# Kernel tuning notes

Measured on AMD Instinct MI355X. Metric: run time of the kernel, lower is better.

Reference implementation:

```python
import jax, jax.numpy as jnp
import numpy as np

V, E, H, T, B, D, L = 32000, 512, 512, 128, 4, 4, 2
C0, C1 = 2000, 10000          # adaptive softmax cutoffs
NT = T - D + 1


def setup_inputs() -> dict:
    key = jax.random.key(0)
    ks = jax.random.split(key, 18)
    s = 0.02
    x = jax.random.randint(ks[0], (B, T), 1, V)
    lengths = jnp.sort(jax.random.randint(ks[1], (B,), D, T + 1))[::-1]
    lengths = lengths.at[0].set(T)
    # graph predictor output: per-layer attention matrices [B, L, T, T]
    G = jax.nn.softmax(jax.random.normal(ks[2], (B, L, T, T)), axis=-1)
    emb = (jax.random.normal(ks[3], (V, E)) * s).at[0].set(0.0)  # padding_idx=0
    enc_w_ih = jax.random.normal(ks[4], (L, 3 * H, H)) * s
    enc_w_hh = jax.random.normal(ks[5], (L, 3 * H, H)) * s
    enc_b_ih = jnp.zeros((L, 3 * H))
    enc_b_hh = jnp.zeros((L, 3 * H))
    dec_w_ih = jax.random.normal(ks[6], (3 * H, E)) * s
    dec_w_hh = jax.random.normal(ks[7], (3 * H, H)) * s
    dec_b_ih = jnp.zeros((3 * H,))
    dec_b_hh = jnp.zeros((3 * H,))
    head_w = jax.random.normal(ks[8], (C0 + 2, H)) * s
    t0_proj = jax.random.normal(ks[9], (H // 4, H)) * s
    t0_out = jax.random.normal(ks[10], (C1 - C0, H // 4)) * s
    t1_proj = jax.random.normal(ks[11], (H // 16, H)) * s
    t1_out = jax.random.normal(ks[12], (V - C1, H // 16)) * s
    return dict(x=x, lengths=lengths, G=G, emb=emb,
                enc_w_ih=enc_w_ih, enc_w_hh=enc_w_hh, enc_b_ih=enc_b_ih, enc_b_hh=enc_b_hh,
                dec_w_ih=dec_w_ih, dec_w_hh=dec_w_hh, dec_b_ih=dec_b_ih, dec_b_hh=dec_b_hh,
                head_w=head_w, t0_proj=t0_proj, t0_out=t0_out, t1_proj=t1_proj, t1_out=t1_out)


def gru_step(xt, h, w_ih, w_hh, b_ih, b_hh):
    """torch nn.GRU/GRUCell math; works on arbitrary leading dims."""
    gi = xt @ w_ih.T + b_ih
    gh = h @ w_hh.T + b_hh
    i_r, i_z, i_n = jnp.split(gi, 3, axis=-1)
    h_r, h_z, h_n = jnp.split(gh, 3, axis=-1)
    r = jax.nn.sigmoid(i_r + h_r)
    z = jax.nn.sigmoid(i_z + h_z)
    n = jnp.tanh(i_n + r * h_n)
    return (1.0 - z) * n + z * h


def adaptive_log_prob(h, head_w, t0_proj, t0_out, t1_proj, t1_out):
    """torch AdaptiveLogSoftmaxWithLoss.log_prob: h [N,H] -> [N,V]."""
    head_lp = jax.nn.log_softmax(h @ head_w.T, axis=-1)                      # [N, C0+2]
    lp0 = head_lp[:, C0:C0 + 1] + jax.nn.log_softmax((h @ t0_proj.T) @ t0_out.T, axis=-1)
    lp1 = head_lp[:, C0 + 1:C0 + 2] + jax.nn.log_softmax((h @ t1_proj.T) @ t1_out.T, axis=-1)
    return jnp.concatenate([head_lp[:, :C0], lp0, lp1], axis=-1)


def reference(x, lengths, G, emb, enc_w_ih, enc_w_hh, enc_b_ih, enc_b_hh,
              dec_w_ih, dec_w_hh, dec_b_ih, dec_b_hh,
              head_w, t0_proj, t0_out, t1_proj, t1_out):
    b = x.shape[0]
    input_f = emb[x]                      # [B,T,E] (dropout p=0)
    embedded = input_f
    # ---- encoder: graph-weighted aggregation + GRUCell per layer ----
    for l in range(enc_w_ih.shape[0]):
        wgt = jnp.einsum('bji,bjd->bid', G[:, l], input_f)   # G_l^T @ input_f
        input_f = gru_step(wgt, input_f, enc_w_ih[l], enc_w_hh[l], enc_b_ih[l], enc_b_hh[l])
    # ---- decoder: length-D GRU window per start position t ----
    t_idx = jnp.arange(NT)
    d_idx = jnp.arange(D)
    tok_idx = jnp.broadcast_to(t_idx[None, :, None] + d_idx[None, None, :] - 1, (b, NT, D))
    tok_idx = tok_idx.at[:, 0, 0].set(lengths - 1)           # t=0,d=0 uses embedded[lengths-1]
    wins = jnp.take_along_axis(embedded, tok_idx.reshape(b, -1)[:, :, None], axis=1)
    wins = wins.reshape(b, NT, D, E)
    h0 = input_f[:, :NT, :]                                  # [B,NT,H]
    def step(h, xd):
        hn = gru_step(xd, h, dec_w_ih, dec_w_hh, dec_b_ih, dec_b_hh)
        return hn, hn
    _, hs = jax.lax.scan(step, h0, jnp.moveaxis(wins, 2, 0))  # [D,B,NT,H]
    hs = jnp.moveaxis(hs, 0, 2)                               # [B,NT,D,H]
    # pad_packed_sequence zeros hidden beyond per-row lens = min(lengths - t, D)
    valid = (t_idx[None, :, None] + d_idx[None, None, :]) < lengths[:, None, None]
    hs = jnp.where(valid[..., None], hs, 0.0)
    lp = adaptive_log_prob(hs.reshape(-1, H), head_w, t0_proj, t0_out, t1_proj, t1_out)
    lp = lp.reshape(b, NT, D, V)
    # batch rows with lengths <= t were excluded and F.pad'ed with zeros
    row_valid = t_idx[None, :] < lengths[:, None]
    lp = jnp.where(row_valid[:, :, None, None], lp, 0.0)
    return lp.reshape(b, NT * D, V)
```

## Files before the change

### kernel.cpp

```cpp
#include <hip/hip_runtime.h>
#include <hip/hip_bf16.h>
#include <hip/hip_fp16.h>

typedef __hip_bfloat16 bf16;
typedef __attribute__((ext_vector_type(8))) short short8v;
typedef __attribute__((ext_vector_type(4))) float float4v;

#define V_    32000
#define E_    512
#define H_    512
#define T_    128
#define B_    4
#define D_    4
#define L_    2
#define C0_   2000
#define C1_   10000
#define NT_   125
#define NROW_ 2000
#define NH_   2002
#define NTOTC 2162
#define NSLOT 252

__device__ __forceinline__ float bf2f(bf16 v) { return __bfloat162float(v); }
__device__ __forceinline__ unsigned short f2bfu(float f) {
    bf16 h = __float2bfloat16(f);
    union { bf16 h; unsigned short u; } cv; cv.h = h; return cv.u;
}
__device__ __forceinline__ float ld1(const void* p, size_t i, int bf) {
    return bf ? bf2f(((const bf16*)p)[i]) : ((const float*)p)[i];
}

__device__ __forceinline__ void lse_push(float z, float& m, float& s) {
    if (z <= m) { s += __expf(z - m); }
    else        { s = s * __expf(m - z) + 1.0f; m = z; }
}
__device__ __forceinline__ void lse_merge(float m2, float s2, float& m, float& s) {
    float mm = fmaxf(m, m2);
    s = s * __expf(m - mm) + s2 * __expf(m2 - mm);
    m = mm;
}

__global__ void k_detect(const void* __restrict__ G, int* __restrict__ flag) {
    int t = threadIdx.x;
    float s32 = 0.0f;
    for (int k = t; k < 128; k += 64) s32 += ((const float*)G)[k];
    for (int off = 32; off; off >>= 1) s32 += __shfl_down(s32, off);
    if (t == 0) {
        float e32 = fabsf(s32 - 1.0f);
        *flag = (e32 < 0.05f) ? 0 : 1;
    }
}

struct ConvArgs {
    const void* src[9];
    unsigned int off[10];
};
__global__ void k_wembed(ConvArgs a, unsigned short* __restrict__ wb,
                         const int* __restrict__ flagp,
                         const int* __restrict__ x, const void* __restrict__ emb,
                         float* __restrict__ embedded, float* __restrict__ f0,
                         unsigned short* __restrict__ f0b) {
    const int bf = *flagp;
    if (blockIdx.x < 1024) {
        int i = blockIdx.x * 256 + threadIdx.x;
        int bt = i >> 9, e = i & 511;
        int tok = x[bt];
        float v = ld1(emb, (size_t)tok * E_ + e, bf);
        embedded[i] = v; f0[i] = v; f0b[i] = f2bfu(v);
    } else {
        unsigned int totalg = a.off[9] >> 2;
        unsigned int stride = (gridDim.x - 1024) * 256;
        for (unsigned int g = (blockIdx.x - 1024) * 256 + threadIdx.x; g < totalg;
             g += stride) {
            unsigned int i = g << 2;
            int seg = 0;
            while (i >= a.off[seg + 1]) seg++;
            unsigned int o = i - a.off[seg];
            unsigned short r[4];
            if (bf) {
                *(uint2*)r = *(const uint2*)((const unsigned short*)a.src[seg] + o);
            } else {
                float4 v = *(const float4*)((const float*)a.src[seg] + o);
                r[0] = f2bfu(v.x); r[1] = f2bfu(v.y);
                r[2] = f2bfu(v.z); r[3] = f2bfu(v.w);
            }
            *(uint2*)(wb + i) = *(const uint2*)r;
        }
    }
}

__global__ void k_wgt(const void* __restrict__ G, const float* __restrict__ f,
                      unsigned short* __restrict__ wgtb, int l,
                      const int* __restrict__ flagp) {
    const int bf = *flagp;
    int i = blockIdx.x * 256 + threadIdx.x;
    int e = i & 511;
    int bi = i >> 9;
    int b = bi >> 7, ip = bi & 127;
    size_t gbase = ((size_t)(b * L_ + l) * T_ * T_) + ip;
    const float* fb = f + (size_t)b * T_ * E_ + e;
    float acc = 0.0f;
    #pragma unroll 4
    for (int j = 0; j < T_; ++j)
        acc = fmaf(ld1(G, gbase + (size_t)j * T_, bf), fb[(size_t)j * E_], acc);
    wgtb[i] = f2bfu(acc);
}

struct GemmP {
    const unsigned short* A0;
    const unsigned short* A1;
    const unsigned short* W;
    unsigned long long w1off;
    int M, N, K, Nlse;
    float* Zg; int ldz; int zcol1;
    const void* bias0; const void* bias1; int boff;
    void* zraw; int outColOff;
    float* stats;
    unsigned short* p0b;
    unsigned short* p1b;
    float* lsep; int slotBase;
    const int* lengths;
    const int* flagp;
    int gx;
};

__device__ __forceinline__ void zstore(void* zraw, size_t i, int bf, float v) {
    if (bf) ((__half*)zraw)[i] = __float2half(v);
    else    ((float*)zraw)[i]  = v;
}

template<int MODE>
__device__ __forceinline__ void gemm_core(const GemmP& p, int bx, int by,
        unsigned short* As, unsigned short* Bs,
        float (*pm)[2], float (*ps)[2]) {
    const int bf = *p.flagp;
    const int zsel = (MODE == 0) ? blockIdx.z : 0;
    const unsigned short* A  = zsel ? p.A1 : p.A0;
    const unsigned short* Bw = p.W + (zsel ? p.w1off : 0ull);
    const int M = p.M, N = p.N, K = p.K;
    const int m0 = by * 128, n0 = bx * 128;
    const int t = threadIdx.x;
    const int wave = t >> 6, lane = t & 63;
    const int wm = wave >> 1, wn = wave & 1;
    const int quad = lane >> 4, l16 = lane & 15;

    float4v acc[4][4];
    #pragma unroll
    for (int mi = 0; mi < 4; ++mi)
        #pragma unroll
        for (int ni = 0; ni < 4; ++ni)
            acc[mi][ni] = (float4v){0.f, 0.f, 0.f, 0.f};

    for (int k0 = 0; k0 < K; k0 += 32) {
        if (k0) __syncthreads();
        #pragma unroll
        for (int i = 0; i < 2; ++i) {
            int idx = t + i * 256;
            int row = idx >> 2, seg = idx & 3;
            uint4 av = {0u, 0u, 0u, 0u};
            int gm = m0 + row;
            if (gm < M) av = *(const uint4*)(A + (size_t)gm * K + k0 + seg * 8);
            *(uint4*)(&As[row * 40 + seg * 8]) = av;
            uint4 bv = {0u, 0u, 0u, 0u};
            int gn = n0 + row;
            if (gn < N) bv = *(const uint4*)(Bw + (size_t)gn * K + k0 + seg * 8);
            *(uint4*)(&Bs[row * 40 + seg * 8]) = bv;
        }
        __syncthreads();
        short8v af[4], bfv[4];
        #pragma unroll
        for (int mi = 0; mi < 4; ++mi)
            af[mi] = *(const short8v*)(As + (wm * 64 + mi * 16 + l16) * 40 + quad * 8);
        #pragma unroll
        for (int ni = 0; ni < 4; ++ni)
            bfv[ni] = *(const short8v*)(Bs + (wn * 64 + ni * 16 + l16) * 40 + quad * 8);
        #pragma unroll
        for (int mi = 0; mi < 4; ++mi)
            #pragma unroll
            for (int ni = 0; ni < 4; ++ni)
                acc[mi][ni] = __builtin_amdgcn_mfma_f32_16x16x32_bf16(
                    af[mi], bfv[ni], acc[mi][ni], 0, 0, 0);
    }

    if (MODE == 0) {
        const void* bias = zsel ? p.bias1 : p.bias0;
        const int zcol = zsel ? p.zcol1 : 0;
        #pragma unroll
        for (int mi = 0; mi < 4; ++mi)
            #pragma unroll
            for (int r = 0; r < 4; ++r) {
                int grow = m0 + wm * 64 + mi * 16 + quad * 4 + r;
                if (grow >= M) continue;
                #pragma unroll
                for (int ni = 0; ni < 4; ++ni) {
                    int gcol = n0 + wn * 64 + ni * 16 + l16;
                    if (gcol < N)
                        p.Zg[(size_t)grow * p.ldz + zcol + gcol] =
                            acc[mi][ni][r] + ld1(bias, p.boff + gcol, bf);
                }
            }
    } else if (MODE == 1) {
        #pragma unroll
        for (int mi = 0; mi < 4; ++mi)
            #pragma unroll
            for (int r = 0; r < 4; ++r) {
                int grow = m0 + wm * 64 + mi * 16 + quad * 4 + r;
                if (grow >= M) continue;
                #pragma unroll
                for (int ni = 0; ni < 4; ++ni) {
                    int gcol = n0 + wn * 64 + ni * 16 + l16;
                    float v = acc[mi][ni][r];
                    if (gcol < C0_) zstore(p.zraw, (size_t)grow * V_ + gcol, bf, v);
                    else if (gcol < NH_) p.stats[grow * 8 + 2 + (gcol - C0_)] = v;
                    else if (gcol < 2130) p.p0b[grow * 128 + (gcol - NH_)] = f2bfu(v);
                    else if (gcol < NTOTC) p.p1b[grow * 32 + (gcol - 2130)] = f2bfu(v);
                }
            }
    } else {
        #pragma unroll
        for (int mi = 0; mi < 4; ++mi)
            #pragma unroll
            for (int r = 0; r < 4; ++r) {
                int grow = m0 + wm * 64 + mi * 16 + quad * 4 + r;
                if (grow >= M) continue;
                #pragma unroll
                for (int ni = 0; ni < 4; ++ni) {
                    int gcol = n0 + wn * 64 + ni * 16 + l16;
                    if (gcol < N)
                        zstore(p.zraw, (size_t)grow * V_ + p.outColOff + gcol, bf,
                               acc[mi][ni][r]);
                }
            }
    }

    if (MODE == 1 || MODE == 2) {
        const int Nlse = p.Nlse;
        #pragma unroll
        for (int mi = 0; mi < 4; ++mi) {
            #pragma unroll
            for (int r = 0; r < 4; ++r) {
                float m = -1e30f, s = 0.0f;
                #pragma unroll
                for (int ni = 0; ni < 4; ++ni) {
                    int gcol = n0 + wn * 64 + ni * 16 + l16;
                    if (gcol < Nlse) lse_push(acc[mi][ni][r], m, s);
                }
                #pragma unroll
                for (int off = 1; off < 16; off <<= 1) {
                    float m2 = __shfl_xor(m, off), s2 = __shfl_xor(s, off);
                    lse_merge(m2, s2, m, s);
                }
                if (l16 == 0) {
                    int rl = wm * 64 + mi * 16 + quad * 4 + r;
                    pm[rl][wn] = m; ps[rl][wn] = s;
                }
            }
        }
        __syncthreads();
        if (t < 128) {
            int grow = m0 + t;
            if (grow < M) {
                float m = pm[t][0], s = ps[t][0];
                lse_merge(pm[t][1], ps[t][1], m, s);
                float* dst = p.lsep + ((size_t)(p.slotBase + bx) * NROW_ + grow) * 2;
                dst[0] = m; dst[1] = s;
            }
        }
    }
}

template<int MODE>
__global__ __launch_bounds__(256, 2) void k_gemm(GemmP p) {
    __shared__ __align__(16) unsigned short As[128 * 40];
    __shared__ __align__(16) unsigned short Bs[128 * 40];
    __shared__ float pm[128][2], ps[128][2];
    gemm_core<MODE>(p, blockIdx.x, blockIdx.y, As, Bs, pm, ps);
}

__global__ __launch_bounds__(256, 2) void k_gemmT(GemmP pa, GemmP pb) {
    __shared__ __align__(16) unsigned short As[128 * 40];
    __shared__ __align__(16) unsigned short Bs[128 * 40];
    __shared__ float pm[128][2], ps[128][2];
    int bx = blockIdx.x;
    if (bx < pa.gx) gemm_core<2>(pa, bx, blockIdx.y, As, Bs, pm, ps);
    else            gemm_core<2>(pb, bx - pa.gx, blockIdx.y, As, Bs, pm, ps);
}

__device__ __forceinline__ float gru2(float i_r, float i_z, float i_n,
                                      float h_r, float h_z, float h_n, float h) {
    float r = 1.0f / (1.0f + __expf(-(i_r + h_r)));
    float z = 1.0f / (1.0f + __expf(-(i_z + h_z)));
    float n = tanhf(i_n + r * h_n);
    return (1.0f - z) * n + z * h;
}

__global__ void k_apply_enc(const float* __restrict__ gates,
                            const float* __restrict__ hprev,
                            float* __restrict__ hnext,
                            unsigned short* __restrict__ hnextb) {
    int i = blockIdx.x * 256 + threadIdx.x;
    int row = i >> 9, k = i & 511;
    const float* g = gates + (size_t)row * 3072;
    float v = gru2(g[k], g[512 + k], g[1024 + k],
                   g[1536 + k], g[2048 + k], g[2560 + k], hprev[i]);
    hnext[i] = v; hnextb[i] = f2bfu(v);
}

__global__ void k_apply_enc2(const float* __restrict__ gates,
                             const float* __restrict__ hprev,
                             float* __restrict__ hnext,
                             unsigned short* __restrict__ hnextb,
                             const float* __restrict__ embedded,
                             const int* __restrict__ lengths,
                             unsigned short* __restrict__ winb,
                             float* __restrict__ hdec,
                             unsigned short* __restrict__ hdecb) {
    int blk = blockIdx.x;
    if (blk < 1024) {
        int i = blk * 256 + threadIdx.x;
        int row = i >> 9, k = i & 511;
        const float* g = gates + (size_t)row * 3072;
        float v = gru2(g[k], g[512 + k], g[1024 + k],
                       g[1536 + k], g[2048 + k], g[2560 + k], hprev[i]);
        hnext[i] = v; hnextb[i] = f2bfu(v);
        int b = row >> 7, t = row & 127;
        if (t < NT_) {
            int j = ((b * NT_ + t) << 9) + k;
            hdec[j] = v; hdecb[j] = f2bfu(v);
        }
    } else {
        int i = (blk - 1024) * 256 + threadIdx.x;
        int e = i & 511;
        int wr = i >> 9;
        int d = wr / 500, row = wr - d * 500;
        int b = row / NT_, t = row - b * NT_;
        int tok = (d == 0 && t == 0) ? (lengths[b] - 1) : (t + d - 1);
        winb[i] = f2bfu(embedded[((size_t)(b * T_ + tok) << 9) + e]);
    }
}

__global__ void k_apply_dec(const float* __restrict__ gih,
                            const float* __restrict__ ghh,
                            float* __restrict__ hdec,
                            unsigned short* __restrict__ hdecb,
                            unsigned short* __restrict__ hsb,
                            const int* __restrict__ lengths, int d) {
    int i = blockIdx.x * 256 + threadIdx.x;
    int row = i >> 9, k = i & 511;
    int b = row / NT_, t = row - b * NT_;
    const float* gi = gih + (size_t)(d * 500 + row) * 1536;
    const float* gh = ghh + (size_t)row * 1536;
    float hn = gru2(gi[k], gi[512 + k], gi[1024 + k],
                    gh[k], gh[512 + k], gh[1024 + k], hdec[i]);
    hdec[i] = hn; hdecb[i] = f2bfu(hn);
    bool valid = (t + d) < lengths[b];
    hsb[(((size_t)row * D_ + d) << 9) + k] = valid ? f2bfu(hn) : (unsigned short)0;
}

__global__ void k_corr2(const float* __restrict__ lsep, const float* __restrict__ stats,
                        float* __restrict__ corr) {
    int r = blockIdx.x * 256 + threadIdx.x;
    if (r >= NROW_) return;
    float m = -1e30f, s = 0.0f;
    for (int i = 0; i < 17; ++i) {
        const float* P = lsep + ((size_t)i * NROW_ + r) * 2;
        lse_merge(P[0], P[1], m, s);
    }
    float ch = m + logf(s);
    float lp0 = stats[r * 8 + 2] - ch;
    float lp1 = stats[r * 8 + 3] - ch;
    m = -1e30f; s = 0.0f;
    for (int i = 17; i < 80; ++i) {
        const float* P = lsep + ((size_t)i * NROW_ + r) * 2;
        lse_merge(P[0], P[1], m, s);
    }
    float ct0 = m + logf(s);
    m = -1e30f; s = 0.0f;
    for (int i = 80; i < 252; ++i) {
        const float* P = lsep + ((size_t)i * NROW_ + r) * 2;
        lse_merge(P[0], P[1], m, s);
    }
    float ct1 = m + logf(s);
    corr[r * 4 + 0] = ch;
    corr[r * 4 + 1] = ct0 - lp0;
    corr[r * 4 + 2] = ct1 - lp1;
}

__global__ void k_fix(const float* __restrict__ corr,
                      const int* __restrict__ lengths, void* __restrict__ out,
                      const int* __restrict__ flagp) {
    const int bf = *flagp;
    int idx = blockIdx.x * 256 + threadIdx.x;
    if (idx >= NROW_ * (V_ / 8)) return;
    int row = idx / (V_ / 8);
    int col = (idx - row * (V_ / 8)) * 8;
    int b = row / 500;
    int tt = (row - b * 500) >> 2;
    bool valid = tt < lengths[b];
    int cri = (col < C0_) ? 0 : (col < C1_ ? 1 : 2);
    float cr = corr[row * 4 + cri];
    size_t base = (size_t)row * V_ + col;
    if (bf) {
        unsigned short* p16 = (unsigned short*)out + base;
        union { uint4 u; __half h[8]; } in;
        in.u = *(const uint4*)p16;
        union { uint4 u; unsigned short s[8]; } o;
        #pragma unroll
        for (int j = 0; j < 8; ++j)
            o.s[j] = f2bfu(valid ? (__half2float(in.h[j]) - cr) : 0.0f);
        *(uint4*)p16 = o.u;
    } else {
        float* op = (float*)out + base;
        float4 a = *(float4*)op, c = *(float4*)(op + 4);
        float4 ra = valid ? (float4){a.x - cr, a.y - cr, a.z - cr, a.w - cr}
                          : (float4){0.f, 0.f, 0.f, 0.f};
        float4 rc = valid ? (float4){c.x - cr, c.y - cr, c.z - cr, c.w - cr}
                          : (float4){0.f, 0.f, 0.f, 0.f};
        *(float4*)op = ra; *(float4*)(op + 4) = rc;
    }
}

#define OFF_EMB    0u
#define OFF_FA     262144u
#define OFF_FB     524288u
#define OFF_FAB    786432u
#define OFF_FBB    917504u
#define OFF_WGTB   1048576u
#define OFF_GATES  1179648u
#define OFF_GIH    2752512u
#define OFF_GHH    5824512u
#define OFF_HDEC   6592512u
#define OFF_HDECB  6848512u
#define OFF_WINB   6976512u
#define OFF_HSB    7488512u
#define OFF_P0B    8000512u
#define OFF_P1B    8128512u
#define OFF_STATS  8160512u
#define OFF_CORR   8176512u
#define OFF_LSEP   8184512u
#define OFF_WB     9192512u
#define OFF_FLAG   12969264u

#define WO_ENCIH   0u
#define WO_ENCHH   1572864u
#define WO_DECIH   3145728u
#define WO_DECHH   3932160u
#define WO_W1      4718592u
#define WO_T0O     5825536u
#define WO_T1O     6849536u
#define WO_END     7553504u

static inline GemmP mkp(const unsigned short* A0, const unsigned short* A1,
                        const unsigned short* W, unsigned long long w1off,
                        int M, int N, int K, int Nlse,
                        float* Zg, int ldz, int zcol1,
                        const void* bias0, const void* bias1, int boff,
                        void* zraw, int outColOff, float* stats,
                        unsigned short* p0b, unsigned short* p1b,
                        float* lsep, int slotBase,
                        const int* lengths, const int* flagp) {
    GemmP p;
    p.A0 = A0; p.A1 = A1; p.W = W; p.w1off = w1off;
    p.M = M; p.N = N; p.K = K; p.Nlse = Nlse;
    p.Zg = Zg; p.ldz = ldz; p.zcol1 = zcol1;
    p.bias0 = bias0; p.bias1 = bias1; p.boff = boff;
    p.zraw = zraw; p.outColOff = outColOff; p.stats = stats;
    p.p0b = p0b; p.p1b = p1b; p.lsep = lsep; p.slotBase = slotBase;
    p.lengths = lengths; p.flagp = flagp; p.gx = 0;
    return p;
}

extern "C" void kernel_launch(void* const* d_in, const int* in_sizes, int n_in,
                              void* d_out, int out_size, void* d_ws, size_t ws_size,
                              hipStream_t stream) {
    (void)in_sizes; (void)n_in; (void)out_size; (void)ws_size;
    const int*  x        = (const int*)d_in[0];
    const int*  lengths  = (const int*)d_in[1];
    const void* G        = d_in[2];
    const void* emb      = d_in[3];
    const void* enc_w_ih = d_in[4];
    const void* enc_w_hh = d_in[5];
    const void* enc_b_ih = d_in[6];
    const void* enc_b_hh = d_in[7];
    const void* dec_w_ih = d_in[8];
    const void* dec_w_hh = d_in[9];
    const void* dec_b_ih = d_in[10];
    const void* dec_b_hh = d_in[11];
    const void* head_w   = d_in[12];
    const void* t0_proj  = d_in[13];
    const void* t0_out   = d_in[14];
    const void* t1_proj  = d_in[15];
    const void* t1_out   = d_in[16];

    float* ws = (float*)d_ws;
    float* embedded = ws + OFF_EMB;
    float* fA    = ws + OFF_FA;
    float* fB    = ws + OFF_FB;
    unsigned short* fAb  = (unsigned short*)(ws + OFF_FAB);
    unsigned short* fBb  = (unsigned short*)(ws + OFF_FBB);
    unsigned short* wgtb = (unsigned short*)(ws + OFF_WGTB);
    float* gates = ws + OFF_GATES;
    float* gih   = ws + OFF_GIH;
    float* ghh   = ws + OFF_GHH;
    float* hdec  = ws + OFF_HDEC;
    unsigned short* hdecb = (unsigned short*)(ws + OFF_HDECB);
    unsigned short* winb  = (unsigned short*)(ws + OFF_WINB);
    unsigned short* hsb   = (unsigned short*)(ws + OFF_HSB);
    unsigned short* p0b   = (unsigned short*)(ws + OFF_P0B);
    unsigned short* p1b   = (unsigned short*)(ws + OFF_P1B);
    float* stats = ws + OFF_STATS;
    float* corr  = ws + OFF_CORR;
    float* lsep  = ws + OFF_LSEP;
    unsigned short* WB = (unsigned short*)(ws + OFF_WB);
    int* flagp = (int*)(ws + OFF_FLAG);
    void* out = d_out;

    k_detect<<<1, 64, 0, stream>>>(G, flagp);

    ConvArgs ca;
    ca.src[0] = enc_w_ih; ca.src[1] = enc_w_hh; ca.src[2] = dec_w_ih;
    ca.src[3] = dec_w_hh; ca.src[4] = head_w;   ca.src[5] = t0_proj;
    ca.src[6] = t1_proj;  ca.src[7] = t0_out;   ca.src[8] = t1_out;
    ca.off[0] = WO_ENCIH; ca.off[1] = WO_ENCHH; ca.off[2] = WO_DECIH;
    ca.off[3] = WO_DECHH; ca.off[4] = WO_W1;
    ca.off[5] = WO_W1 + 2002u * 512u;
    ca.off[6] = WO_W1 + 2130u * 512u;
    ca.off[7] = WO_T0O;   ca.off[8] = WO_T1O;   ca.off[9] = WO_END;
    k_wembed<<<3072, 256, 0, stream>>>(ca, WB, flagp, x, emb, embedded, fA, fAb);

    k_wgt<<<1024, 256, 0, stream>>>(G, fA, wgtb, 0, flagp);
    k_gemm<0><<<dim3(12, 4, 2), 256, 0, stream>>>(mkp(
        wgtb, fAb, WB + WO_ENCIH, (unsigned long long)(WO_ENCHH - WO_ENCIH),
        512, 1536, 512, 0, gates, 3072, 1536, enc_b_ih, enc_b_hh, 0,
        nullptr, 0, nullptr, nullptr, nullptr, nullptr, 0, lengths, flagp));
    k_apply_enc<<<1024, 256, 0, stream>>>(gates, fA, fB, fBb);

    k_wgt<<<1024, 256, 0, stream>>>(G, fB, wgtb, 1, flagp);
    k_gemm<0><<<dim3(12, 4, 2), 256, 0, stream>>>(mkp(
        wgtb, fBb, WB + WO_ENCIH + 786432u, (unsigned long long)(WO_ENCHH - WO_ENCIH),
        512, 1536, 512, 0, gates, 3072, 1536, enc_b_ih, enc_b_hh, 1536,
        nullptr, 0, nullptr, nullptr, nullptr, nullptr, 0, lengths, flagp));
    k_apply_enc2<<<5024, 256, 0, stream>>>(gates, fB, fA, fAb, embedded, lengths,
                                           winb, hdec, hdecb);

    k_gemm<0><<<dim3(12, 16, 1), 256, 0, stream>>>(mkp(
        winb, nullptr, WB + WO_DECIH, 0ull, 2000, 1536, 512, 0,
        gih, 1536, 0, dec_b_ih, nullptr, 0,
        nullptr, 0, nullptr, nullptr, nullptr, nullptr, 0, lengths, flagp));

    for (int d = 0; d < D_; ++d) {
        k_gemm<0><<<dim3(12, 4, 1), 256, 0, stream>>>(mkp(
            hdecb, nullptr, WB + WO_DECHH, 0ull, 500, 1536, 512, 0,
            ghh, 1536, 0, dec_b_hh, nullptr, 0,
            nullptr, 0, nullptr, nullptr, nullptr, nullptr, 0, lengths, flagp));
        k_apply_dec<<<1000, 256, 0, stream>>>(gih, ghh, hdec, hdecb, hsb, lengths, d);
    }

    k_gemm<1><<<dim3(17, 16, 1), 256, 0, stream>>>(mkp(
        hsb, nullptr, WB + WO_W1, 0ull, NROW_, NTOTC, 512, NH_,
        nullptr, 0, 0, nullptr, nullptr, 0, out, 0,
        stats, p0b, p1b, lsep, 0, lengths, flagp));
    {
        GemmP pa = mkp(p0b, nullptr, WB + WO_T0O, 0ull, NROW_, 8000, 128, 8000,
                       nullptr, 0, 0, nullptr, nullptr, 0, out, C0_,
                       stats, nullptr, nullptr, lsep, 17, lengths, flagp);
        pa.gx = 63;
        GemmP pb = mkp(p1b, nullptr, WB + WO_T1O, 0ull, NROW_, 22000, 32, 22000,
                       nullptr, 0, 0, nullptr, nullptr, 0, out, C1_,
                       stats, nullptr, nullptr, lsep, 80, lengths, flagp);
        pb.gx = 172;
        k_gemmT<<<dim3(235, 16, 1), 256, 0, stream>>>(pa, pb);
    }

    k_corr2<<<8, 256, 0, stream>>>(lsep, stats, corr);

    k_fix<<<31250, 256, 0, stream>>>(corr, lengths, out, flagp);
}
```

Measured before the change: 765.8 us.

## Fold dtype detect, head GEMM and LSE correction into neighbouring kernels

Removes the separate dtype-detect kernel by computing the flag inside each k_wembed block. Splits the head GEMM so that a small GEMM produces only the tail projections, then runs the head-logit GEMM alongside both tail GEMMs in one three-way launch. Drops k_corr2 by having each k_fix block reduce the log-sum-exp partials for its rows with wave shuffles. This saves launches and serialisation, at the cost of redundant detection work per block and repeated per-block LSE reductions.

```diff
diff --git a/kernel.cpp b/kernel.cpp
--- a/kernel.cpp
+++ b/kernel.cpp
@@ -18,8 +18,9 @@
 #define NT_   125
 #define NROW_ 2000
 #define NH_   2002
-#define NTOTC 2162
 #define NSLOT 252
+#define SB_T0 16
+#define SB_T1 79
 
 __device__ __forceinline__ float bf2f(bf16 v) { return __bfloat162float(v); }
 __device__ __forceinline__ unsigned short f2bfu(float f) {
@@ -38,17 +39,6 @@
     float mm = fmaxf(m, m2);
     s = s * __expf(m - mm) + s2 * __expf(m2 - mm);
     m = mm;
-}
-
-__global__ void k_detect(const void* __restrict__ G, int* __restrict__ flag) {
-    int t = threadIdx.x;
-    float s32 = 0.0f;
-    for (int k = t; k < 128; k += 64) s32 += ((const float*)G)[k];
-    for (int off = 32; off; off >>= 1) s32 += __shfl_down(s32, off);
-    if (t == 0) {
-        float e32 = fabsf(s32 - 1.0f);
-        *flag = (e32 < 0.05f) ? 0 : 1;
-    }
 }
 
 struct ConvArgs {
@@ -56,11 +46,23 @@
     unsigned int off[10];
 };
 __global__ void k_wembed(ConvArgs a, unsigned short* __restrict__ wb,
-                         const int* __restrict__ flagp,
+                         int* __restrict__ flagp,
                          const int* __restrict__ x, const void* __restrict__ emb,
                          float* __restrict__ embedded, float* __restrict__ f0,
-                         unsigned short* __restrict__ f0b) {
-    const int bf = *flagp;
+                         unsigned short* __restrict__ f0b,
+                         const void* __restrict__ G) {
+    __shared__ int s_bf;
+    if (threadIdx.x < 64) {
+        float s32 = ((const float*)G)[threadIdx.x] + ((const float*)G)[threadIdx.x + 64];
+        for (int off = 32; off; off >>= 1) s32 += __shfl_down(s32, off);
+        if (threadIdx.x == 0) {
+            int v = (fabsf(s32 - 1.0f) < 0.05f) ? 0 : 1;
+            s_bf = v;
+            if (blockIdx.x == 0) *flagp = v;
+        }
+    }
+    __syncthreads();
+    const int bf = s_bf;
     if (blockIdx.x < 1024) {
         int i = blockIdx.x * 256 + threadIdx.x;
         int bt = i >> 9, e = i & 511;
@@ -212,11 +214,9 @@
                     float v = acc[mi][ni][r];
                     if (gcol < C0_) zstore(p.zraw, (size_t)grow * V_ + gcol, bf, v);
                     else if (gcol < NH_) p.stats[grow * 8 + 2 + (gcol - C0_)] = v;
-                    else if (gcol < 2130) p.p0b[grow * 128 + (gcol - NH_)] = f2bfu(v);
-                    else if (gcol < NTOTC) p.p1b[grow * 32 + (gcol - 2130)] = f2bfu(v);
                 }
             }
-    } else {
+    } else if (MODE == 2) {
         #pragma unroll
         for (int mi = 0; mi < 4; ++mi)
             #pragma unroll
@@ -229,6 +229,21 @@
                     if (gcol < N)
                         zstore(p.zraw, (size_t)grow * V_ + p.outColOff + gcol, bf,
                                acc[mi][ni][r]);
+                }
+            }
+    } else {
+        #pragma unroll
+        for (int mi = 0; mi < 4; ++mi)
+            #pragma unroll
+            for (int r = 0; r < 4; ++r) {
+                int grow = m0 + wm * 64 + mi * 16 + quad * 4 + r;
+                if (grow >= M) continue;
+                #pragma unroll
+                for (int ni = 0; ni < 4; ++ni) {
+                    int gcol = n0 + wn * 64 + ni * 16 + l16;
+                    float v = acc[mi][ni][r];
+                    if (gcol < 128) p.p0b[grow * 128 + gcol] = f2bfu(v);
+                    else if (gcol < 160) p.p1b[grow * 32 + (gcol - 128)] = f2bfu(v);
                 }
             }
     }
@@ -277,13 +292,14 @@
     gemm_core<MODE>(p, blockIdx.x, blockIdx.y, As, Bs, pm, ps);
 }
 
-__global__ __launch_bounds__(256, 2) void k_gemmT(GemmP pa, GemmP pb) {
+__global__ __launch_bounds__(256, 2) void k_gemmT3(GemmP pa, GemmP pb, GemmP pc) {
     __shared__ __align__(16) unsigned short As[128 * 40];
     __shared__ __align__(16) unsigned short Bs[128 * 40];
     __shared__ float pm[128][2], ps[128][2];
     int bx = blockIdx.x;
-    if (bx < pa.gx) gemm_core<2>(pa, bx, blockIdx.y, As, Bs, pm, ps);
-    else            gemm_core<2>(pb, bx - pa.gx, blockIdx.y, As, Bs, pm, ps);
+    if (bx < pa.gx)              gemm_core<1>(pa, bx, blockIdx.y, As, Bs, pm, ps);
+    else if (bx < pa.gx + pb.gx) gemm_core<2>(pb, bx - pa.gx, blockIdx.y, As, Bs, pm, ps);
+    else                         gemm_core<2>(pc, bx - pa.gx - pb.gx, blockIdx.y, As, Bs, pm, ps);
 }
 
 __device__ __forceinline__ float gru2(float i_r, float i_z, float i_n,
@@ -357,48 +373,55 @@
     hsb[(((size_t)row * D_ + d) << 9) + k] = valid ? f2bfu(hn) : (unsigned short)0;
 }
 
-__global__ void k_corr2(const float* __restrict__ lsep, const float* __restrict__ stats,
-                        float* __restrict__ corr) {
-    int r = blockIdx.x * 256 + threadIdx.x;
-    if (r >= NROW_) return;
-    float m = -1e30f, s = 0.0f;
-    for (int i = 0; i < 17; ++i) {
-        const float* P = lsep + ((size_t)i * NROW_ + r) * 2;
-        lse_merge(P[0], P[1], m, s);
-    }
-    float ch = m + logf(s);
-    float lp0 = stats[r * 8 + 2] - ch;
-    float lp1 = stats[r * 8 + 3] - ch;
-    m = -1e30f; s = 0.0f;
-    for (int i = 17; i < 80; ++i) {
-        const float* P = lsep + ((size_t)i * NROW_ + r) * 2;
-        lse_merge(P[0], P[1], m, s);
-    }
-    float ct0 = m + logf(s);
-    m = -1e30f; s = 0.0f;
-    for (int i = 80; i < 252; ++i) {
-        const float* P = lsep + ((size_t)i * NROW_ + r) * 2;
-        lse_merge(P[0], P[1], m, s);
-    }
-    float ct1 = m + logf(s);
-    corr[r * 4 + 0] = ch;
-    corr[r * 4 + 1] = ct0 - lp0;
-    corr[r * 4 + 2] = ct1 - lp1;
-}
-
-__global__ void k_fix(const float* __restrict__ corr,
+__global__ void k_fix(const float* __restrict__ lsep, const float* __restrict__ stats,
                       const int* __restrict__ lengths, void* __restrict__ out,
                       const int* __restrict__ flagp) {
     const int bf = *flagp;
-    int idx = blockIdx.x * 256 + threadIdx.x;
-    if (idx >= NROW_ * (V_ / 8)) return;
-    int row = idx / (V_ / 8);
-    int col = (idx - row * (V_ / 8)) * 8;
+    const int GPR = V_ / 8;
+    int firstIdx = blockIdx.x * 256;
+    int row0 = firstIdx / GPR;
+    int rowLast = (firstIdx + 255) / GPR;
+    __shared__ float scorr[2][4];
+    int w = threadIdx.x >> 6, lane = threadIdx.x & 63;
+    if (w <= rowLast - row0 && w < 2) {
+        int r = row0 + w;
+        float mh = -1e30f, sh = 0.f, m0 = -1e30f, s0 = 0.f, m1 = -1e30f, s1 = 0.f;
+        if (lane < 16) {
+            const float* P = lsep + ((size_t)lane * NROW_ + r) * 2;
+            mh = P[0]; sh = P[1];
+        }
+        if (lane < 63) {
+            const float* P = lsep + ((size_t)(SB_T0 + lane) * NROW_ + r) * 2;
+            m0 = P[0]; s0 = P[1];
+        }
+        for (int j = lane; j < 172; j += 64) {
+            const float* P = lsep + ((size_t)(SB_T1 + j) * NROW_ + r) * 2;
+            lse_merge(P[0], P[1], m1, s1);
+        }
+        #pragma unroll
+        for (int off = 32; off; off >>= 1) {
+            lse_merge(__shfl_xor(mh, off), __shfl_xor(sh, off), mh, sh);
+            lse_merge(__shfl_xor(m0, off), __shfl_xor(s0, off), m0, s0);
+            lse_merge(__shfl_xor(m1, off), __shfl_xor(s1, off), m1, s1);
+        }
+        if (lane == 0) {
+            float ch  = mh + logf(sh);
+            float ct0 = m0 + logf(s0);
+            float ct1 = m1 + logf(s1);
+            scorr[w][0] = ch;
+            scorr[w][1] = ct0 - (stats[r * 8 + 2] - ch);
+            scorr[w][2] = ct1 - (stats[r * 8 + 3] - ch);
+        }
+    }
+    __syncthreads();
+    int idx = firstIdx + threadIdx.x;
+    int row = idx / GPR;
+    int col = (idx - row * GPR) * 8;
     int b = row / 500;
     int tt = (row - b * 500) >> 2;
     bool valid = tt < lengths[b];
     int cri = (col < C0_) ? 0 : (col < C1_ ? 1 : 2);
-    float cr = corr[row * 4 + cri];
+    float cr = scorr[row - row0][cri];
     size_t base = (size_t)row * V_ + col;
     if (bf) {
         unsigned short* p16 = (unsigned short*)out + base;
@@ -436,7 +459,6 @@
 #define OFF_P0B    8000512u
 #define OFF_P1B    8128512u
 #define OFF_STATS  8160512u
-#define OFF_CORR   8176512u
 #define OFF_LSEP   8184512u
 #define OFF_WB     9192512u
 #define OFF_FLAG   12969264u
@@ -509,13 +531,10 @@
     unsigned short* p0b   = (unsigned short*)(ws + OFF_P0B);
     unsigned short* p1b   = (unsigned short*)(ws + OFF_P1B);
     float* stats = ws + OFF_STATS;
-    float* corr  = ws + OFF_CORR;
     float* lsep  = ws + OFF_LSEP;
     unsigned short* WB = (unsigned short*)(ws + OFF_WB);
     int* flagp = (int*)(ws + OFF_FLAG);
     void* out = d_out;
-
-    k_detect<<<1, 64, 0, stream>>>(G, flagp);
 
     ConvArgs ca;
     ca.src[0] = enc_w_ih; ca.src[1] = enc_w_hh; ca.src[2] = dec_w_ih;
@@ -526,7 +545,7 @@
     ca.off[5] = WO_W1 + 2002u * 512u;
     ca.off[6] = WO_W1 + 2130u * 512u;
     ca.off[7] = WO_T0O;   ca.off[8] = WO_T1O;   ca.off[9] = WO_END;
-    k_wembed<<<3072, 256, 0, stream>>>(ca, WB, flagp, x, emb, embedded, fA, fAb);
+    k_wembed<<<3072, 256, 0, stream>>>(ca, WB, flagp, x, emb, embedded, fA, fAb, G);
 
     k_wgt<<<1024, 256, 0, stream>>>(G, fA, wgtb, 0, flagp);
     k_gemm<0><<<dim3(12, 4, 2), 256, 0, stream>>>(mkp(
@@ -556,23 +575,26 @@
         k_apply_dec<<<1000, 256, 0, stream>>>(gih, ghh, hdec, hdecb, hsb, lengths, d);
     }
 
-    k_gemm<1><<<dim3(17, 16, 1), 256, 0, stream>>>(mkp(
-        hsb, nullptr, WB + WO_W1, 0ull, NROW_, NTOTC, 512, NH_,
-        nullptr, 0, 0, nullptr, nullptr, 0, out, 0,
-        stats, p0b, p1b, lsep, 0, lengths, flagp));
+    k_gemm<3><<<dim3(2, 16, 1), 256, 0, stream>>>(mkp(
+        hsb, nullptr, WB + WO_W1 + 2002u * 512u, 0ull, NROW_, 160, 512, 0,
+        nullptr, 0, 0, nullptr, nullptr, 0, nullptr, 0,
+        nullptr, p0b, p1b, nullptr, 0, lengths, flagp));
+
     {
-        GemmP pa = mkp(p0b, nullptr, WB + WO_T0O, 0ull, NROW_, 8000, 128, 8000,
+        GemmP pa = mkp(hsb, nullptr, WB + WO_W1, 0ull, NROW_, NH_, 512, NH_,
+                       nullptr, 0, 0, nullptr, nullptr, 0, out, 0,
+                       stats, nullptr, nullptr, lsep, 0, lengths, flagp);
+        pa.gx = 16;
+        GemmP pb = mkp(p0b, nullptr, WB + WO_T0O, 0ull, NROW_, 8000, 128, 8000,
                        nullptr, 0, 0, nullptr, nullptr, 0, out, C0_,
-                       stats, nullptr, nullptr, lsep, 17, lengths, flagp);
-        pa.gx = 63;
-        GemmP pb = mkp(p1b, nullptr, WB + WO_T1O, 0ull, NROW_, 22000, 32, 22000,
+                       stats, nullptr, nullptr, lsep, SB_T0, lengths, flagp);
+        pb.gx = 63;
+        GemmP pc = mkp(p1b, nullptr, WB + WO_T1O, 0ull, NROW_, 22000, 32, 22000,
                        nullptr, 0, 0, nullptr, nullptr, 0, out, C1_,
-                       stats, nullptr, nullptr, lsep, 80, lengths, flagp);
-        pb.gx = 172;
-        k_gemmT<<<dim3(235, 16, 1), 256, 0, stream>>>(pa, pb);
-    }
-
-    k_corr2<<<8, 256, 0, stream>>>(lsep, stats, corr);
-
-    k_fix<<<31250, 256, 0, stream>>>(corr, lengths, out, flagp);
-}
+                       stats, nullptr, nullptr, lsep, SB_T1, lengths, flagp);
+        pc.gx = 172;
+        k_gemmT3<<<dim3(251, 16, 1), 256, 0, stream>>>(pa, pb, pc);
+    }
+
+    k_fix<<<31250, 256, 0, stream>>>(lsep, stats, lengths, out, flagp);
+}
```

Measured after the change: 862.6 us. 12.6% more time.
